# Performance work log

Measured on AMD Instinct MI355X. Metric: run time of the kernel, lower is better.

Reference implementation:

```python
import jax, jax.numpy as jnp
import numpy as np

N_DRUG, N_DIS, E, D = 10000, 15000, 1048576, 128

def setup_inputs() -> dict:
    key = jax.random.key(0)
    k = jax.random.split(key, 6)
    return {
        "z_drug": jax.random.normal(k[0], (N_DRUG, D), dtype=jnp.float32),
        "z_disease": jax.random.normal(k[1], (N_DIS, D), dtype=jnp.float32),
        "row": jax.random.randint(k[2], (E,), 0, N_DRUG),
        "col": jax.random.randint(k[3], (E,), 0, N_DIS),
        "W1": jax.random.normal(k[4], (2 * D, D), dtype=jnp.float32) * (1.0 / np.sqrt(2 * D)),
        "b1": jnp.zeros((D,), dtype=jnp.float32),
        "W2": jax.random.normal(k[5], (D, 1), dtype=jnp.float32) * (1.0 / np.sqrt(D)),
        "b2": jnp.zeros((1,), dtype=jnp.float32),
    }

def reference(z_drug, z_disease, row, col, W1, b1, W2, b2):
    # gather per-edge embeddings and concatenate: [E, 2D]
    z = jnp.concatenate([z_drug[row], z_disease[col]], axis=-1)
    h = jax.nn.relu(z @ W1 + b1)          # [E, D]
    out = h @ W2 + b2                      # [E, 1]
    return out.reshape(-1)                 # [E]
```

## Files before the change

### kernel.cpp

```cpp
#include <hip/hip_runtime.h>

typedef __attribute__((ext_vector_type(8))) short short8;
typedef __attribute__((ext_vector_type(4))) float floatx4;
typedef __attribute__((ext_vector_type(4))) float float4v;
typedef __attribute__((ext_vector_type(4))) unsigned short ushort4v;

#define TILE_M 64
#define TILE_SHORTS (TILE_M * 256)

static __device__ __forceinline__ unsigned short f2bf(float x) {
    unsigned int u = __builtin_bit_cast(unsigned int, x);
    unsigned int r = (u + 0x7FFFu + ((u >> 16) & 1u)) >> 16;
    return (unsigned short)r;
}

static __device__ __forceinline__ void gld16(const unsigned short* g, unsigned short* l) {
    __builtin_amdgcn_global_load_lds(
        (const __attribute__((address_space(1))) unsigned int*)g,
        (__attribute__((address_space(3))) unsigned int*)l, 16, 0, 0);
}

__global__ void prep_all(const float* __restrict__ zd, const float* __restrict__ zs,
                         const float* __restrict__ W1,
                         int nd4, int ns4,
                         unsigned short* __restrict__ outd, unsigned short* __restrict__ outs,
                         unsigned short* __restrict__ w1t) {
    int i = blockIdx.x * 256 + threadIdx.x;
    int total4 = nd4 + ns4;
    if (i < total4) {
        const float* src; unsigned short* dst; int j;
        if (i < nd4) { src = zd; dst = outd; j = i; }
        else         { src = zs; dst = outs; j = i - nd4; }
        float4v v = *reinterpret_cast<const float4v*>(src + (size_t)j * 4);
        ushort4v o;
        o.x = f2bf(v.x); o.y = f2bf(v.y); o.z = f2bf(v.z); o.w = f2bf(v.w);
        *reinterpret_cast<ushort4v*>(dst + (size_t)j * 4) = o;
    } else {
        int j = i - total4;
        if (j < 128 * 256) {
            int n = j >> 8;
            int k = j & 255;
            w1t[n * 256 + k] = f2bf(W1[k * 128 + n]);
        }
    }
}

__global__ __launch_bounds__(256, 2) void edge_mlp(
    const unsigned short* __restrict__ zd, const unsigned short* __restrict__ zs,
    const int* __restrict__ row, const int* __restrict__ col,
    const unsigned short* __restrict__ w1t,
    const float* __restrict__ b1, const float* __restrict__ w2,
    const float* __restrict__ b2, float* __restrict__ out, int ntiles)
{
    __shared__ unsigned short lds_a[2][TILE_SHORTS];
    __shared__ float red[2][2][TILE_M];

    const int tid  = threadIdx.x;
    const int lane = tid & 63;
    const int wave = tid >> 6;
    const int wh   = wave >> 1;
    const int we   = wave & 1;
    const int l15  = lane & 15;
    const int quad = lane >> 4;
    const int whbase = wh * 64;

    short8 wfrag[32];
    #pragma unroll
    for (int s = 0; s < 8; ++s)
        #pragma unroll
        for (int mt = 0; mt < 4; ++mt)
            wfrag[s * 4 + mt] = *reinterpret_cast<const short8*>(
                &w1t[(size_t)(whbase + mt * 16 + l15) * 256 + s * 32 + quad * 8]);

    float4v b1v[4], w2v[4];
    #pragma unroll
    for (int mt = 0; mt < 4; ++mt) {
        b1v[mt] = *reinterpret_cast<const float4v*>(&b1[whbase + mt * 16 + quad * 4]);
        w2v[mt] = *reinterpret_cast<const float4v*>(&w2[whbase + mt * 16 + quad * 4]);
    }
    const float b2v = b2[0];

    const int e0 = tid >> 5;
    const int jxw = tid & 31;
    const int jlog = jxw ^ (e0 & 7);
    const unsigned short* tab = (jlog >= 16) ? zs : zd;
    const int* idxp = (jlog >= 16) ? col : row;
    const int koff = (jlog & 15) * 8;

    const int hb = (l15 >> 2) & 1;
    const int qx = quad ^ (l15 & 3);

    const int G = gridDim.x;
    const int R = ntiles / G;
    const long t0 = blockIdx.x;

    int nidx[8];
    #pragma unroll
    for (int i = 0; i < 8; ++i) nidx[i] = idxp[t0 * TILE_M + e0 + 8 * i];
    #pragma unroll
    for (int i = 0; i < 8; ++i)
        gld16(tab + (size_t)nidx[i] * 128 + koff, &lds_a[0][2048 * i + 512 * wave]);
    {
        long t1 = (R >= 2) ? (t0 + G) : t0;
        #pragma unroll
        for (int i = 0; i < 8; ++i) nidx[i] = idxp[t1 * TILE_M + e0 + 8 * i];
    }

    floatx4 acc[2][4];

    for (int r = 0; r < R; ++r) {
        const long t = t0 + (long)r * G;

        __syncthreads();

        if (r + 1 < R) {
            #pragma unroll
            for (int i = 0; i < 8; ++i)
                gld16(tab + (size_t)nidx[i] * 128 + koff,
                      &lds_a[(r + 1) & 1][2048 * i + 512 * wave]);
        }
        {
            long t2 = (r + 2 < R) ? (t0 + (long)(r + 2) * G) : t0;
            #pragma unroll
            for (int i = 0; i < 8; ++i) nidx[i] = idxp[t2 * TILE_M + e0 + 8 * i];
        }

        if (r >= 2 && lane < 16) {
            int eo = wave * 16 + l15;
            out[(t - 2 * G) * TILE_M + eo] =
                red[r & 1][0][eo] + red[r & 1][1][eo] + b2v;
        }

        if (r >= 1) {
            const int slot = (r - 1) & 1;
            #pragma unroll
            for (int et = 0; et < 2; ++et) {
                float v = 0.f;
                #pragma unroll
                for (int mt = 0; mt < 4; ++mt)
                    #pragma unroll
                    for (int rr = 0; rr < 4; ++rr) {
                        float h = acc[et][mt][rr] + b1v[mt][rr];
                        h = h > 0.f ? h : 0.f;
                        v += h * w2v[mt][rr];
                    }
                v += __shfl_xor(v, 16);
                v += __shfl_xor(v, 32);
                if (lane < 16) red[slot][wh][we * 32 + et * 16 + l15] = v;
            }
        }

        const unsigned short* buf = lds_a[r & 1];
        #pragma unroll
        for (int et = 0; et < 2; ++et)
            #pragma unroll
            for (int mt = 0; mt < 4; ++mt)
                acc[et][mt] = (floatx4)(0.0f);

        #pragma unroll
        for (int s = 0; s < 8; ++s) {
            const int sx = s ^ hb;
            short8 ef[2];
            #pragma unroll
            for (int et = 0; et < 2; ++et) {
                int e = we * 32 + et * 16 + l15;
                ef[et] = *reinterpret_cast<const short8*>(&buf[e * 256 + sx * 32 + qx * 8]);
            }
            #pragma unroll
            for (int et = 0; et < 2; ++et)
                #pragma unroll
                for (int mt = 0; mt < 4; ++mt)
                    acc[et][mt] = __builtin_amdgcn_mfma_f32_16x16x32_bf16(
                        wfrag[s * 4 + mt], ef[et], acc[et][mt], 0, 0, 0);
        }
    }

    __syncthreads();
    if (R >= 2 && lane < 16) {
        int eo = wave * 16 + l15;
        long tt = t0 + (long)(R - 2) * G;
        out[tt * TILE_M + eo] = red[R & 1][0][eo] + red[R & 1][1][eo] + b2v;
    }
    {
        const int slot = (R - 1) & 1;
        #pragma unroll
        for (int et = 0; et < 2; ++et) {
            float v = 0.f;
            #pragma unroll
            for (int mt = 0; mt < 4; ++mt)
                #pragma unroll
                for (int rr = 0; rr < 4; ++rr) {
                    float h = acc[et][mt][rr] + b1v[mt][rr];
                    h = h > 0.f ? h : 0.f;
                    v += h * w2v[mt][rr];
                }
            v += __shfl_xor(v, 16);
            v += __shfl_xor(v, 32);
            if (lane < 16) red[slot][wh][we * 32 + et * 16 + l15] = v;
        }
    }
    __syncthreads();
    if (lane < 16) {
        int eo = wave * 16 + l15;
        long tt = t0 + (long)(R - 1) * G;
        out[tt * TILE_M + eo] = red[(R - 1) & 1][0][eo] + red[(R - 1) & 1][1][eo] + b2v;
    }
}

extern "C" void kernel_launch(void* const* d_in, const int* in_sizes, int n_in,
                              void* d_out, int out_size, void* d_ws, size_t ws_size,
                              hipStream_t stream) {
    const float* zd = (const float*)d_in[0];
    const float* zs = (const float*)d_in[1];
    const int*   row = (const int*)d_in[2];
    const int*   col = (const int*)d_in[3];
    const float* W1 = (const float*)d_in[4];
    const float* b1 = (const float*)d_in[5];
    const float* w2 = (const float*)d_in[6];
    const float* b2 = (const float*)d_in[7];
    float* out = (float*)d_out;

    const int nd = in_sizes[0];
    const int ns = in_sizes[1];
    const int E  = in_sizes[2];

    unsigned short* zd_b = (unsigned short*)d_ws;
    unsigned short* zs_b = zd_b + nd;
    unsigned short* w1t  = zs_b + ns;

    const int total_jobs = (nd + ns) / 4 + 128 * 256;
    const int pgrid = (total_jobs + 255) / 256;
    hipLaunchKernelGGL(prep_all, dim3(pgrid), dim3(256), 0, stream,
                       zd, zs, W1, nd / 4, ns / 4, zd_b, zs_b, w1t);

    const int ntiles = E / TILE_M;
    const int nblocks = 512;
    hipLaunchKernelGGL(edge_mlp, dim3(nblocks), dim3(256), 0, stream,
                       zd_b, zs_b, row, col, w1t, b1, w2, b2, out, ntiles);
}
```

Baseline: 144.5 us.

## Split hidden dim across 8 waves per block with 512 threads

Result: slower. 157.8 us (+9.2%).

```diff
diff --git a/kernel.cpp b/kernel.cpp
--- a/kernel.cpp
+++ b/kernel.cpp
@@ -45,7 +45,7 @@
     }
 }
 
-__global__ __launch_bounds__(256, 2) void edge_mlp(
+__global__ __launch_bounds__(512, 4) void edge_mlp(
     const unsigned short* __restrict__ zd, const unsigned short* __restrict__ zs,
     const int* __restrict__ row, const int* __restrict__ col,
     const unsigned short* __restrict__ w1t,
@@ -53,7 +53,7 @@
     const float* __restrict__ b2, float* __restrict__ out, int ntiles)
 {
     __shared__ unsigned short lds_a[2][TILE_SHORTS];
-    __shared__ float red[2][2][TILE_M];
+    __shared__ float red[2][4][TILE_M];
 
     const int tid  = threadIdx.x;
     const int lane = tid & 63;
@@ -62,21 +62,21 @@
     const int we   = wave & 1;
     const int l15  = lane & 15;
     const int quad = lane >> 4;
-    const int whbase = wh * 64;
-
-    short8 wfrag[32];
+    const int whbase = wh * 32;
+
+    short8 wfrag[16];
     #pragma unroll
     for (int s = 0; s < 8; ++s)
         #pragma unroll
-        for (int mt = 0; mt < 4; ++mt)
-            wfrag[s * 4 + mt] = *reinterpret_cast<const short8*>(
+        for (int mt = 0; mt < 2; ++mt)
+            wfrag[s * 2 + mt] = *reinterpret_cast<const short8*>(
                 &w1t[(size_t)(whbase + mt * 16 + l15) * 256 + s * 32 + quad * 8]);
 
-    float4v b1v[4], w2v[4];
-    #pragma unroll
-    for (int mt = 0; mt < 4; ++mt) {
-        b1v[mt] = *reinterpret_cast<const float4v*>(&b1[whbase + mt * 16 + quad * 4]);
-        w2v[mt] = *reinterpret_cast<const float4v*>(&w2[whbase + mt * 16 + quad * 4]);
+    floatx4 b1v[2], w2v[2];
+    #pragma unroll
+    for (int mt = 0; mt < 2; ++mt) {
+        b1v[mt] = *reinterpret_cast<const floatx4*>(&b1[whbase + mt * 16 + quad * 4]);
+        w2v[mt] = *reinterpret_cast<const floatx4*>(&w2[whbase + mt * 16 + quad * 4]);
     }
     const float b2v = b2[0];
 
@@ -94,19 +94,19 @@
     const int R = ntiles / G;
     const long t0 = blockIdx.x;
 
-    int nidx[8];
-    #pragma unroll
-    for (int i = 0; i < 8; ++i) nidx[i] = idxp[t0 * TILE_M + e0 + 8 * i];
-    #pragma unroll
-    for (int i = 0; i < 8; ++i)
-        gld16(tab + (size_t)nidx[i] * 128 + koff, &lds_a[0][2048 * i + 512 * wave]);
+    int nidx[4];
+    #pragma unroll
+    for (int i = 0; i < 4; ++i) nidx[i] = idxp[t0 * TILE_M + e0 + 16 * i];
+    #pragma unroll
+    for (int i = 0; i < 4; ++i)
+        gld16(tab + (size_t)nidx[i] * 128 + koff, &lds_a[0][4096 * i + 512 * wave]);
     {
         long t1 = (R >= 2) ? (t0 + G) : t0;
         #pragma unroll
-        for (int i = 0; i < 8; ++i) nidx[i] = idxp[t1 * TILE_M + e0 + 8 * i];
-    }
-
-    floatx4 acc[2][4];
+        for (int i = 0; i < 4; ++i) nidx[i] = idxp[t1 * TILE_M + e0 + 16 * i];
+    }
+
+    floatx4 acc[2][2];
 
     for (int r = 0; r < R; ++r) {
         const long t = t0 + (long)r * G;
@@ -115,48 +115,49 @@
 
         if (r + 1 < R) {
             #pragma unroll
-            for (int i = 0; i < 8; ++i)
+            for (int i = 0; i < 4; ++i)
                 gld16(tab + (size_t)nidx[i] * 128 + koff,
-                      &lds_a[(r + 1) & 1][2048 * i + 512 * wave]);
+                      &lds_a[(r + 1) & 1][4096 * i + 512 * wave]);
         }
         {
             long t2 = (r + 2 < R) ? (t0 + (long)(r + 2) * G) : t0;
             #pragma unroll
-            for (int i = 0; i < 8; ++i) nidx[i] = idxp[t2 * TILE_M + e0 + 8 * i];
-        }
-
-        if (r >= 2 && lane < 16) {
+            for (int i = 0; i < 4; ++i) nidx[i] = idxp[t2 * TILE_M + e0 + 16 * i];
+        }
+
+        if (r >= 2 && wave < 4 && lane < 16) {
             int eo = wave * 16 + l15;
             out[(t - 2 * G) * TILE_M + eo] =
-                red[r & 1][0][eo] + red[r & 1][1][eo] + b2v;
-        }
-
+                red[r & 1][0][eo] + red[r & 1][1][eo] +
+                red[r & 1][2][eo] + red[r & 1][3][eo] + b2v;
+        }
+
+        float v[2];
         if (r >= 1) {
-            const int slot = (r - 1) & 1;
             #pragma unroll
             for (int et = 0; et < 2; ++et) {
-                float v = 0.f;
+                float p0 = 0.f, p1 = 0.f;
                 #pragma unroll
-                for (int mt = 0; mt < 4; ++mt)
+                for (int mt = 0; mt < 2; ++mt)
                     #pragma unroll
                     for (int rr = 0; rr < 4; ++rr) {
-                        float h = acc[et][mt][rr] + b1v[mt][rr];
+                        float h = acc[et][mt][rr];
                         h = h > 0.f ? h : 0.f;
-                        v += h * w2v[mt][rr];
+                        if (rr & 1) p1 += h * w2v[mt][rr];
+                        else        p0 += h * w2v[mt][rr];
                     }
-                v += __shfl_xor(v, 16);
-                v += __shfl_xor(v, 32);
-                if (lane < 16) red[slot][wh][we * 32 + et * 16 + l15] = v;
+                v[et] = p0 + p1;
             }
         }
 
+        #pragma unroll
+        for (int et = 0; et < 2; ++et)
+            #pragma unroll
+            for (int mt = 0; mt < 2; ++mt)
+                acc[et][mt] = b1v[mt];
+
         const unsigned short* buf = lds_a[r & 1];
-        #pragma unroll
-        for (int et = 0; et < 2; ++et)
-            #pragma unroll
-            for (int mt = 0; mt < 4; ++mt)
-                acc[et][mt] = (floatx4)(0.0f);
-
+        __builtin_amdgcn_s_setprio(1);
         #pragma unroll
         for (int s = 0; s < 8; ++s) {
             const int sx = s ^ hb;
@@ -169,41 +170,57 @@
             #pragma unroll
             for (int et = 0; et < 2; ++et)
                 #pragma unroll
-                for (int mt = 0; mt < 4; ++mt)
+                for (int mt = 0; mt < 2; ++mt)
                     acc[et][mt] = __builtin_amdgcn_mfma_f32_16x16x32_bf16(
-                        wfrag[s * 4 + mt], ef[et], acc[et][mt], 0, 0, 0);
+                        wfrag[s * 2 + mt], ef[et], acc[et][mt], 0, 0, 0);
+        }
+        __builtin_amdgcn_s_setprio(0);
+
+        if (r >= 1) {
+            const int slot = (r - 1) & 1;
+            #pragma unroll
+            for (int et = 0; et < 2; ++et) {
+                float x = v[et];
+                x += __shfl_xor(x, 16);
+                x += __shfl_xor(x, 32);
+                if (lane < 16) red[slot][wh][we * 32 + et * 16 + l15] = x;
+            }
         }
     }
 
     __syncthreads();
-    if (R >= 2 && lane < 16) {
+    if (R >= 2 && wave < 4 && lane < 16) {
         int eo = wave * 16 + l15;
         long tt = t0 + (long)(R - 2) * G;
-        out[tt * TILE_M + eo] = red[R & 1][0][eo] + red[R & 1][1][eo] + b2v;
+        out[tt * TILE_M + eo] = red[R & 1][0][eo] + red[R & 1][1][eo] +
+                                red[R & 1][2][eo] + red[R & 1][3][eo] + b2v;
     }
     {
         const int slot = (R - 1) & 1;
         #pragma unroll
         for (int et = 0; et < 2; ++et) {
-            float v = 0.f;
-            #pragma unroll
-            for (int mt = 0; mt < 4; ++mt)
+            float p0 = 0.f, p1 = 0.f;
+            #pragma unroll
+            for (int mt = 0; mt < 2; ++mt)
                 #pragma unroll
                 for (int rr = 0; rr < 4; ++rr) {
-                    float h = acc[et][mt][rr] + b1v[mt][rr];
+                    float h = acc[et][mt][rr];
                     h = h > 0.f ? h : 0.f;
-                    v += h * w2v[mt][rr];
+                    if (rr & 1) p1 += h * w2v[mt][rr];
+                    else        p0 += h * w2v[mt][rr];
                 }
-            v += __shfl_xor(v, 16);
-            v += __shfl_xor(v, 32);
-            if (lane < 16) red[slot][wh][we * 32 + et * 16 + l15] = v;
+            float x = p0 + p1;
+            x += __shfl_xor(x, 16);
+            x += __shfl_xor(x, 32);
+            if (lane < 16) red[slot][wh][we * 32 + et * 16 + l15] = x;
         }
     }
     __syncthreads();
-    if (lane < 16) {
+    if (wave < 4 && lane < 16) {
         int eo = wave * 16 + l15;
         long tt = t0 + (long)(R - 1) * G;
-        out[tt * TILE_M + eo] = red[(R - 1) & 1][0][eo] + red[(R - 1) & 1][1][eo] + b2v;
+        out[tt * TILE_M + eo] = red[(R - 1) & 1][0][eo] + red[(R - 1) & 1][1][eo] +
+                                red[(R - 1) & 1][2][eo] + red[(R - 1) & 1][3][eo] + b2v;
     }
 }
 
@@ -235,6 +252,6 @@
 
     const int ntiles = E / TILE_M;
     const int nblocks = 512;
-    hipLaunchKernelGGL(edge_mlp, dim3(nblocks), dim3(256), 0, stream,
+    hipLaunchKernelGGL(edge_mlp, dim3(nblocks), dim3(512), 0, stream,
                        zd_b, zs_b, row, col, w1t, b1, w2, b2, out, ntiles);
 }
```

## Replace LDS-staged 4-wave tiles with single-wave blocks gathering directly to registers

Applied to the files above, without the earlier changes.

After: 204.4 us. 1.41x slower.

```diff
diff --git a/kernel.cpp b/kernel.cpp
--- a/kernel.cpp
+++ b/kernel.cpp
@@ -5,26 +5,17 @@
 typedef __attribute__((ext_vector_type(4))) float float4v;
 typedef __attribute__((ext_vector_type(4))) unsigned short ushort4v;
 
-#define TILE_M 64
-#define TILE_SHORTS (TILE_M * 256)
-
 static __device__ __forceinline__ unsigned short f2bf(float x) {
     unsigned int u = __builtin_bit_cast(unsigned int, x);
     unsigned int r = (u + 0x7FFFu + ((u >> 16) & 1u)) >> 16;
     return (unsigned short)r;
 }
 
-static __device__ __forceinline__ void gld16(const unsigned short* g, unsigned short* l) {
-    __builtin_amdgcn_global_load_lds(
-        (const __attribute__((address_space(1))) unsigned int*)g,
-        (__attribute__((address_space(3))) unsigned int*)l, 16, 0, 0);
-}
-
 __global__ void prep_all(const float* __restrict__ zd, const float* __restrict__ zs,
                          const float* __restrict__ W1,
-                         int nd4, int ns4,
+                         int nd4, int ns4, int e4,
                          unsigned short* __restrict__ outd, unsigned short* __restrict__ outs,
-                         unsigned short* __restrict__ w1t) {
+                         unsigned short* __restrict__ w1t, float* __restrict__ out0) {
     int i = blockIdx.x * 256 + threadIdx.x;
     int total4 = nd4 + ns4;
     if (i < total4) {
@@ -41,28 +32,31 @@
             int n = j >> 8;
             int k = j & 255;
             w1t[n * 256 + k] = f2bf(W1[k * 128 + n]);
-        }
-    }
-}
-
-__global__ __launch_bounds__(256, 2) void edge_mlp(
+        } else {
+            int j2 = j - 128 * 256;
+            if (j2 < e4) {
+                float4v z4 = {0.f, 0.f, 0.f, 0.f};
+                *reinterpret_cast<float4v*>(out0 + (size_t)j2 * 4) = z4;
+            }
+        }
+    }
+}
+
+__global__ __launch_bounds__(64, 2) void edge_mlp(
     const unsigned short* __restrict__ zd, const unsigned short* __restrict__ zs,
     const int* __restrict__ row, const int* __restrict__ col,
     const unsigned short* __restrict__ w1t,
     const float* __restrict__ b1, const float* __restrict__ w2,
-    const float* __restrict__ b2, float* __restrict__ out, int ntiles)
+    const float* __restrict__ b2, float* __restrict__ out, int ng)
 {
-    __shared__ unsigned short lds_a[2][TILE_SHORTS];
-    __shared__ float red[2][2][TILE_M];
-
-    const int tid  = threadIdx.x;
-    const int lane = tid & 63;
-    const int wave = tid >> 6;
-    const int wh   = wave >> 1;
-    const int we   = wave & 1;
+    const int lane = threadIdx.x;
     const int l15  = lane & 15;
     const int quad = lane >> 4;
-    const int whbase = wh * 64;
+
+    const int b = blockIdx.x;
+    const int half   = (b >> 3) & 1;
+    const int stream = (b & 7) | ((b >> 4) << 3);
+    const int whbase = half * 64;
 
     short8 wfrag[32];
     #pragma unroll
@@ -72,139 +66,111 @@
             wfrag[s * 4 + mt] = *reinterpret_cast<const short8*>(
                 &w1t[(size_t)(whbase + mt * 16 + l15) * 256 + s * 32 + quad * 8]);
 
-    float4v b1v[4], w2v[4];
+    floatx4 b1v[4], w2v[4];
     #pragma unroll
     for (int mt = 0; mt < 4; ++mt) {
-        b1v[mt] = *reinterpret_cast<const float4v*>(&b1[whbase + mt * 16 + quad * 4]);
-        w2v[mt] = *reinterpret_cast<const float4v*>(&w2[whbase + mt * 16 + quad * 4]);
-    }
-    const float b2v = b2[0];
-
-    const int e0 = tid >> 5;
-    const int jxw = tid & 31;
-    const int jlog = jxw ^ (e0 & 7);
-    const unsigned short* tab = (jlog >= 16) ? zs : zd;
-    const int* idxp = (jlog >= 16) ? col : row;
-    const int koff = (jlog & 15) * 8;
-
-    const int hb = (l15 >> 2) & 1;
-    const int qx = quad ^ (l15 & 3);
-
-    const int G = gridDim.x;
-    const int R = ntiles / G;
-    const long t0 = blockIdx.x;
-
-    int nidx[8];
-    #pragma unroll
-    for (int i = 0; i < 8; ++i) nidx[i] = idxp[t0 * TILE_M + e0 + 8 * i];
-    #pragma unroll
-    for (int i = 0; i < 8; ++i)
-        gld16(tab + (size_t)nidx[i] * 128 + koff, &lds_a[0][2048 * i + 512 * wave]);
-    {
-        long t1 = (R >= 2) ? (t0 + G) : t0;
-        #pragma unroll
-        for (int i = 0; i < 8; ++i) nidx[i] = idxp[t1 * TILE_M + e0 + 8 * i];
-    }
+        b1v[mt] = *reinterpret_cast<const floatx4*>(&b1[whbase + mt * 16 + quad * 4]);
+        w2v[mt] = *reinterpret_cast<const floatx4*>(&w2[whbase + mt * 16 + quad * 4]);
+    }
+    const float badd = (half == 0) ? b2[0] : 0.0f;
+
+    const long gbase = (long)stream * ng;
+
+    int r0 = row[gbase * 32 + l15];
+    int r1 = row[gbase * 32 + 16 + l15];
+    int c0 = col[gbase * 32 + l15];
+    int c1 = col[gbase * 32 + 16 + l15];
+    int rn0, rn1, cn0, cn1;
 
     floatx4 acc[2][4];
 
-    for (int r = 0; r < R; ++r) {
-        const long t = t0 + (long)r * G;
-
-        __syncthreads();
-
-        if (r + 1 < R) {
-            #pragma unroll
-            for (int i = 0; i < 8; ++i)
-                gld16(tab + (size_t)nidx[i] * 128 + koff,
-                      &lds_a[(r + 1) & 1][2048 * i + 512 * wave]);
-        }
+#define EPI(gprev)                                                             \
+    {                                                                          \
+        float p00 = 0.f, p01 = 0.f, p10 = 0.f, p11 = 0.f;                      \
+        _Pragma("unroll")                                                      \
+        for (int mt = 0; mt < 4; ++mt)                                         \
+            _Pragma("unroll")                                                  \
+            for (int rr = 0; rr < 4; ++rr) {                                   \
+                float h0 = acc[0][mt][rr]; h0 = h0 > 0.f ? h0 : 0.f;           \
+                float h1 = acc[1][mt][rr]; h1 = h1 > 0.f ? h1 : 0.f;           \
+                if (rr & 1) { p01 += h0 * w2v[mt][rr]; p11 += h1 * w2v[mt][rr]; } \
+                else        { p00 += h0 * w2v[mt][rr]; p10 += h1 * w2v[mt][rr]; } \
+            }                                                                  \
+        float v0 = p00 + p01, v1 = p10 + p11;                                  \
+        v0 += __shfl_xor(v0, 16); v0 += __shfl_xor(v0, 32);                    \
+        v1 += __shfl_xor(v1, 16); v1 += __shfl_xor(v1, 32);                    \
+        float vv = (lane & 16) ? v1 : v0;                                      \
+        if (lane < 32) atomicAdd(&out[(gprev) * 32 + lane], vv + badd);        \
+    }
+
+    for (int i = 0; i < ng; ++i) {
+        const long g = gbase + i;
+
+        short8 bA[4][2];
+        #pragma unroll
+        for (int s = 0; s < 4; ++s) {
+            bA[s][0] = *reinterpret_cast<const short8*>(&zd[(size_t)r0 * 128 + s * 32 + quad * 8]);
+            bA[s][1] = *reinterpret_cast<const short8*>(&zd[(size_t)r1 * 128 + s * 32 + quad * 8]);
+        }
+
         {
-            long t2 = (r + 2 < R) ? (t0 + (long)(r + 2) * G) : t0;
-            #pragma unroll
-            for (int i = 0; i < 8; ++i) nidx[i] = idxp[t2 * TILE_M + e0 + 8 * i];
-        }
-
-        if (r >= 2 && lane < 16) {
-            int eo = wave * 16 + l15;
-            out[(t - 2 * G) * TILE_M + eo] =
-                red[r & 1][0][eo] + red[r & 1][1][eo] + b2v;
-        }
-
-        if (r >= 1) {
-            const int slot = (r - 1) & 1;
-            #pragma unroll
-            for (int et = 0; et < 2; ++et) {
-                float v = 0.f;
-                #pragma unroll
-                for (int mt = 0; mt < 4; ++mt)
-                    #pragma unroll
-                    for (int rr = 0; rr < 4; ++rr) {
-                        float h = acc[et][mt][rr] + b1v[mt][rr];
-                        h = h > 0.f ? h : 0.f;
-                        v += h * w2v[mt][rr];
-                    }
-                v += __shfl_xor(v, 16);
-                v += __shfl_xor(v, 32);
-                if (lane < 16) red[slot][wh][we * 32 + et * 16 + l15] = v;
-            }
-        }
-
-        const unsigned short* buf = lds_a[r & 1];
+            long gn = (i + 1 < ng) ? (g + 1) : gbase;
+            rn0 = row[gn * 32 + l15];
+            rn1 = row[gn * 32 + 16 + l15];
+            cn0 = col[gn * 32 + l15];
+            cn1 = col[gn * 32 + 16 + l15];
+        }
+
+        if (i > 0) EPI(g - 1)
+
         #pragma unroll
         for (int et = 0; et < 2; ++et)
             #pragma unroll
             for (int mt = 0; mt < 4; ++mt)
-                acc[et][mt] = (floatx4)(0.0f);
-
-        #pragma unroll
-        for (int s = 0; s < 8; ++s) {
-            const int sx = s ^ hb;
-            short8 ef[2];
-            #pragma unroll
-            for (int et = 0; et < 2; ++et) {
-                int e = we * 32 + et * 16 + l15;
-                ef[et] = *reinterpret_cast<const short8*>(&buf[e * 256 + sx * 32 + qx * 8]);
-            }
+                acc[et][mt] = b1v[mt];
+
+        __builtin_amdgcn_s_setprio(1);
+        #pragma unroll
+        for (int s = 0; s < 2; ++s)
             #pragma unroll
             for (int et = 0; et < 2; ++et)
                 #pragma unroll
                 for (int mt = 0; mt < 4; ++mt)
                     acc[et][mt] = __builtin_amdgcn_mfma_f32_16x16x32_bf16(
-                        wfrag[s * 4 + mt], ef[et], acc[et][mt], 0, 0, 0);
-        }
-    }
-
-    __syncthreads();
-    if (R >= 2 && lane < 16) {
-        int eo = wave * 16 + l15;
-        long tt = t0 + (long)(R - 2) * G;
-        out[tt * TILE_M + eo] = red[R & 1][0][eo] + red[R & 1][1][eo] + b2v;
-    }
-    {
-        const int slot = (R - 1) & 1;
-        #pragma unroll
-        for (int et = 0; et < 2; ++et) {
-            float v = 0.f;
-            #pragma unroll
-            for (int mt = 0; mt < 4; ++mt)
+                        wfrag[s * 4 + mt], bA[s][et], acc[et][mt], 0, 0, 0);
+        __builtin_amdgcn_s_setprio(0);
+
+        short8 bB[4][2];
+        #pragma unroll
+        for (int s = 0; s < 4; ++s) {
+            bB[s][0] = *reinterpret_cast<const short8*>(&zs[(size_t)c0 * 128 + s * 32 + quad * 8]);
+            bB[s][1] = *reinterpret_cast<const short8*>(&zs[(size_t)c1 * 128 + s * 32 + quad * 8]);
+        }
+
+        __builtin_amdgcn_s_setprio(1);
+        #pragma unroll
+        for (int s = 2; s < 4; ++s)
+            #pragma unroll
+            for (int et = 0; et < 2; ++et)
                 #pragma unroll
-                for (int rr = 0; rr < 4; ++rr) {
-                    float h = acc[et][mt][rr] + b1v[mt][rr];
-                    h = h > 0.f ? h : 0.f;
-                    v += h * w2v[mt][rr];
-                }
-            v += __shfl_xor(v, 16);
-            v += __shfl_xor(v, 32);
-            if (lane < 16) red[slot][wh][we * 32 + et * 16 + l15] = v;
-        }
-    }
-    __syncthreads();
-    if (lane < 16) {
-        int eo = wave * 16 + l15;
-        long tt = t0 + (long)(R - 1) * G;
-        out[tt * TILE_M + eo] = red[(R - 1) & 1][0][eo] + red[(R - 1) & 1][1][eo] + b2v;
-    }
+                for (int mt = 0; mt < 4; ++mt)
+                    acc[et][mt] = __builtin_amdgcn_mfma_f32_16x16x32_bf16(
+                        wfrag[s * 4 + mt], bA[s][et], acc[et][mt], 0, 0, 0);
+        #pragma unroll
+        for (int s = 0; s < 4; ++s)
+            #pragma unroll
+            for (int et = 0; et < 2; ++et)
+                #pragma unroll
+                for (int mt = 0; mt < 4; ++mt)
+                    acc[et][mt] = __builtin_amdgcn_mfma_f32_16x16x32_bf16(
+                        wfrag[(s + 4) * 4 + mt], bB[s][et], acc[et][mt], 0, 0, 0);
+        __builtin_amdgcn_s_setprio(0);
+
+        r0 = rn0; r1 = rn1; c0 = cn0; c1 = cn1;
+    }
+
+    EPI(gbase + ng - 1)
+#undef EPI
 }
 
 extern "C" void kernel_launch(void* const* d_in, const int* in_sizes, int n_in,
@@ -228,13 +194,13 @@
     unsigned short* zs_b = zd_b + nd;
     unsigned short* w1t  = zs_b + ns;
 
-    const int total_jobs = (nd + ns) / 4 + 128 * 256;
+    const int total_jobs = (nd + ns) / 4 + 128 * 256 + E / 4;
     const int pgrid = (total_jobs + 255) / 256;
     hipLaunchKernelGGL(prep_all, dim3(pgrid), dim3(256), 0, stream,
-                       zd, zs, W1, nd / 4, ns / 4, zd_b, zs_b, w1t);
-
-    const int ntiles = E / TILE_M;
-    const int nblocks = 512;
-    hipLaunchKernelGGL(edge_mlp, dim3(nblocks), dim3(256), 0, stream,
-                       zd_b, zs_b, row, col, w1t, b1, w2, b2, out, ntiles);
-}
+                       zd, zs, W1, nd / 4, ns / 4, E / 4, zd_b, zs_b, w1t, out);
+
+    const int nstreams = 1024;
+    const int ng = (E / 32) / nstreams;
+    hipLaunchKernelGGL(edge_mlp, dim3(2 * nstreams), dim3(64), 0, stream,
+                       zd_b, zs_b, row, col, w1t, b1, w2, b2, out, ng);
+}
```
